# Kernel tuning notes

Hardware: AMD Instinct MI355X
Metric: run time of the kernel (lower is better)

## Reference

```python
import jax, jax.numpy as jnp
import numpy as np

B, N, DIM, H = 4, 2048, 64, 8
SCALE = DIM ** -0.5  # qk_scale defaults to head_dim**-0.5 with head_dim = dim


def setup_inputs() -> dict:
    key = jax.random.key(0)
    k1, k2, k3 = jax.random.split(key, 3)
    x = jax.random.normal(k1, (B, N, DIM), dtype=jnp.float32)
    Wqkv = jax.random.normal(k2, (DIM, 3 * H * DIM), dtype=jnp.float32) * (DIM ** -0.5)
    Wproj = jax.random.normal(k3, (H * DIM, DIM), dtype=jnp.float32) * ((H * DIM) ** -0.5)
    bproj = jnp.zeros((DIM,), dtype=jnp.float32)
    return {"x": x, "Wqkv": Wqkv, "Wproj": Wproj, "bproj": bproj}


def reference(x, Wqkv, Wproj, bproj):
    Bx, Nx, C = x.shape
    # qkv: [B,N,3*H*C] -> [B,N,3,H,C] -> (3,B,H,N,C)
    qkv = (x @ Wqkv).reshape(Bx, Nx, 3, H, C).transpose(2, 0, 3, 1, 4)
    q, k, v = qkv[0], qkv[1], qkv[2]
    # scores: [B,H,N,N]
    attn = jax.nn.softmax(jnp.einsum('bhnc,bhmc->bhnm', q, k) * SCALE, axis=-1)
    out = jnp.einsum('bhnm,bhmc->bhnc', attn, v)  # [B,H,N,C]
    out = out.transpose(0, 2, 1, 3).reshape(Bx, Nx, H * C)  # [B,N,H*C]
    return out @ Wproj + bproj  # [B,N,C]
```

## Files before the change

kernel.cpp:

```cpp
#include <hip/hip_runtime.h>

#define NB 4
#define SEQ 2048
#define CD 64
#define NHEAD 8
#define BHN (NB * NHEAD)
#define ROWS (NB * SEQ)
#define HC 512

#define QSCALE 0.18033688011112042f
#define SHIFT  23.083120654223414f

typedef float f32x4 __attribute__((ext_vector_type(4)));
typedef short s16x8 __attribute__((ext_vector_type(8)));
typedef unsigned short u16;
typedef unsigned int u32;

__device__ __forceinline__ u16 f2bf(float x) {
  union { float f; unsigned u; } v; v.f = x;
  unsigned r = v.u + 0x7FFFu + ((v.u >> 16) & 1u);
  return (u16)(r >> 16);
}

__device__ __forceinline__ float fast_exp2(float x) {
#if __has_builtin(__builtin_amdgcn_exp2f)
  return __builtin_amdgcn_exp2f(x);
#else
  return exp2f(x);
#endif
}

__device__ __forceinline__ u32 bitsf(float x) {
  union { float f; u32 u; } v; v.f = x; return v.u;
}

__device__ __forceinline__ u32 pack_trunc(float a, float b) {
#if __has_builtin(__builtin_amdgcn_perm)
  return __builtin_amdgcn_perm(bitsf(b), bitsf(a), 0x07060302u);
#else
  return (bitsf(a) >> 16) | (bitsf(b) & 0xFFFF0000u);
#endif
}

__device__ __forceinline__ f32x4 mfma_bf16(s16x8 a, s16x8 b, f32x4 c) {
  return __builtin_amdgcn_mfma_f32_16x16x32_bf16(a, b, c, 0, 0, 0);
}

typedef __attribute__((address_space(1))) const u32* gp1;
typedef __attribute__((address_space(3))) u32* lp3;
__device__ __forceinline__ void dma16(const void* g, void* l) {
  __builtin_amdgcn_global_load_lds((gp1)g, (lp3)l, 16, 0, 0);
}

__global__ void __launch_bounds__(256) prep_kernel(
    const float* __restrict__ Wqkv, const float* __restrict__ Wproj,
    u16* __restrict__ WT, u16* __restrict__ WpT) {
  const int idx = blockIdx.x * 256 + threadIdx.x;
  if (idx < 64 * 1536) {
    const int k = idx / 1536, n = idx % 1536;
    WT[n * CD + k] = f2bf(Wqkv[idx]);
  }
  if (idx < 512 * 64) {
    const int k = idx >> 6, c = idx & 63;
    WpT[c * HC + k] = f2bf(Wproj[idx]);
  }
}

__global__ void __launch_bounds__(256) qkv_kernel(
    const float* __restrict__ x, const u16* __restrict__ WT,
    u16* __restrict__ Q, u16* __restrict__ K, u16* __restrict__ Vt) {
  __shared__ __align__(16) u16 xs[64 * 72];
  __shared__ __align__(16) u16 wts[192 * 72];

  const int t = threadIdx.x;
  const int w = t >> 6, lane = t & 63, quad = lane >> 4, c16 = lane & 15;
  const int rb = blockIdx.x * 64;
  const int c0 = blockIdx.y * 192;

  {
    const int row = t >> 2, cc0 = (t & 3) * 16;
    const float* xp = x + (size_t)(rb + row) * CD + cc0;
    union { u16 u[16]; int4 v[2]; } bx;
#pragma unroll
    for (int j = 0; j < 16; j += 4) {
      float4 xv = *(const float4*)(xp + j);
      bx.u[j] = f2bf(xv.x); bx.u[j + 1] = f2bf(xv.y);
      bx.u[j + 2] = f2bf(xv.z); bx.u[j + 3] = f2bf(xv.w);
    }
    *(int4*)&xs[row * 72 + cc0] = bx.v[0];
    *(int4*)&xs[row * 72 + cc0 + 8] = bx.v[1];
  }
#pragma unroll
  for (int pass = 0; pass < 3; ++pass) {
    const int row = pass * 64 + (t >> 2), cc0 = (t & 3) * 16;
    const u16* src = WT + (size_t)(c0 + row) * CD + cc0;
    *(int4*)&wts[row * 72 + cc0] = *(const int4*)src;
    *(int4*)&wts[row * 72 + cc0 + 8] = *(const int4*)(src + 8);
  }
  __syncthreads();

  s16x8 af[2];
#pragma unroll
  for (int kc = 0; kc < 2; ++kc)
    af[kc] = *(const s16x8*)&xs[(w * 16 + c16) * 72 + kc * 32 + quad * 8];

  f32x4 acc[12];
#pragma unroll
  for (int nb = 0; nb < 12; ++nb) acc[nb] = (f32x4){0.f, 0.f, 0.f, 0.f};

#pragma unroll
  for (int nb = 0; nb < 12; ++nb) {
#pragma unroll
    for (int kc = 0; kc < 2; ++kc) {
      const s16x8 bf_ =
          *(const s16x8*)&wts[(nb * 16 + c16) * 72 + kc * 32 + quad * 8];
      acc[nb] = mfma_bf16(af[kc], bf_, acc[nb]);
    }
  }

  const int rw = rb + w * 16;
  const int b = rw >> 11;
  const int nn0 = rw & (SEQ - 1);
#pragma unroll
  for (int nb = 0; nb < 12; ++nb) {
    const int cb = c0 + nb * 16;
    const int three = cb >> 9;
    const int h = (cb >> 6) & 7;
    const int ccb = cb & 63;
    const int bhv = b * NHEAD + h;
    if (three == 2) {
      union { u16 u[4]; uint2 v; } pk;
#pragma unroll
      for (int i = 0; i < 4; ++i) pk.u[i] = f2bf(acc[nb][i]);
      const size_t off = (size_t)bhv * (SEQ * CD) + (size_t)(nn0 >> 5) * 2048 +
                         (size_t)(ccb + c16) * 32 + (rw & 31) + quad * 4;
      *(uint2*)(Vt + off) = pk.v;
    } else {
      u16* dstp = (three == 0) ? Q : K;
      const float scl = (three == 0) ? QSCALE : 1.0f;
#pragma unroll
      for (int i = 0; i < 4; ++i) {
        const int nn = nn0 + quad * 4 + i;
        dstp[((size_t)bhv * SEQ + nn) * CD + ccb + c16] = f2bf(acc[nb][i] * scl);
      }
    }
  }
}

__global__ void __launch_bounds__(128, 2) attn_kernel(
    const u16* __restrict__ Q, const u16* __restrict__ K,
    const u16* __restrict__ Vt, u16* __restrict__ O) {
  __shared__ __align__(16) u16 smem[17664];

  const int t = threadIdx.x;
  const int w = t >> 6, lane = t & 63, quad = lane >> 4, c16 = lane & 15;
  const int bh = blockIdx.y;
  const int q0 = blockIdx.x * 64;
  const int kt0 = w * (SEQ / 2);

  u16* KsW = smem + w * 8192;
  u16* VsW = smem + w * 8192 + 4096;
  u16* Pw  = smem + 16384 + w * 640;

  const u16* Qb = Q + (size_t)bh * SEQ * CD;
  const u16* Kb = K + (size_t)bh * SEQ * CD;
  const u16* Vb = Vt + (size_t)bh * SEQ * CD;

  s16x8 qfb[4][2];
#pragma unroll
  for (int qb = 0; qb < 4; ++qb)
#pragma unroll
    for (int cc = 0; cc < 2; ++cc)
      qfb[qb][cc] = *(const s16x8*)(Qb + (size_t)(q0 + qb * 16 + c16) * CD +
                                    cc * 32 + quad * 8);

  s16x8 onesf;
  {
    const short one = (c16 == 0) ? (short)0x3F80 : (short)0;
#pragma unroll
    for (int j = 0; j < 8; ++j) onesf[j] = one;
  }

  f32x4 o[4][4], osum[4];
#pragma unroll
  for (int qb = 0; qb < 4; ++qb) {
    osum[qb] = (f32x4){0.f, 0.f, 0.f, 0.f};
#pragma unroll
    for (int cb = 0; cb < 4; ++cb) o[qb][cb] = (f32x4){0.f, 0.f, 0.f, 0.f};
  }

  const int krl = lane >> 3, kcl = (lane & 7) ^ ((lane >> 3) & 7);
  const int vrl = lane >> 2, vcl = (lane & 3) ^ ((lane >> 3) & 3);

  int kOff[2][2], vOff[4];
#pragma unroll
  for (int kb = 0; kb < 2; ++kb)
#pragma unroll
    for (int cc = 0; cc < 2; ++cc)
      kOff[kb][cc] = (kb * 16 + c16) * 64 + (((cc * 4 + quad) ^ (c16 & 7)) * 8);
#pragma unroll
  for (int cb = 0; cb < 4; ++cb)
    vOff[cb] = (cb * 16 + c16) * 32 + ((quad ^ ((c16 >> 1) & 3)) * 8);

#define STAGE_TILE(buf_, kt_)                                                  \
  {                                                                            \
    const u16* ksrc = Kb + (size_t)(kt_) * CD;                                 \
    _Pragma("unroll") for (int d = 0; d < 4; ++d)                              \
        dma16(ksrc + (size_t)(d * 8 + krl) * CD + kcl * 8,                     \
              KsW + (buf_) * 2048 + d * 512);                                  \
    const u16* vsrc = Vb + (size_t)((kt_) >> 5) * 2048;                        \
    _Pragma("unroll") for (int d = 0; d < 4; ++d)                              \
        dma16(vsrc + (size_t)(d * 16 + vrl) * 32 + vcl * 8,                    \
              VsW + (buf_) * 2048 + d * 512);                                  \
  }

  STAGE_TILE(0, kt0)

  for (int it = 0; it < 32; ++it) {
    const int bs = it & 1;
    __syncthreads();

    if (it + 1 < 32) STAGE_TILE(bs ^ 1, kt0 + (it + 1) * 32)

    s16x8 kf[2][2], vf[4];
#pragma unroll
    for (int kb = 0; kb < 2; ++kb)
#pragma unroll
      for (int cc = 0; cc < 2; ++cc)
        kf[kb][cc] = *(const s16x8*)&KsW[bs * 2048 + kOff[kb][cc]];
#pragma unroll
    for (int cb = 0; cb < 4; ++cb)
      vf[cb] = *(const s16x8*)&VsW[bs * 2048 + vOff[cb]];

#pragma unroll
    for (int qb = 0; qb < 4; ++qb) {
#pragma unroll
      for (int kb = 0; kb < 2; ++kb) {
        f32x4 s = (f32x4){-SHIFT, -SHIFT, -SHIFT, -SHIFT};
        s = mfma_bf16(kf[kb][0], qfb[qb][0], s);
        s = mfma_bf16(kf[kb][1], qfb[qb][1], s);
        uint2 pk;
        pk.x = pack_trunc(fast_exp2(s[0]), fast_exp2(s[1]));
        pk.y = pack_trunc(fast_exp2(s[2]), fast_exp2(s[3]));
        *(uint2*)&Pw[c16 * 40 + kb * 16 + quad * 4] = pk;
      }
      const s16x8 pf = *(const s16x8*)&Pw[c16 * 40 + quad * 8];
#pragma unroll
      for (int cb = 0; cb < 4; ++cb)
        o[qb][cb] = mfma_bf16(pf, vf[cb], o[qb][cb]);
      osum[qb] = mfma_bf16(pf, onesf, osum[qb]);
    }
  }
#undef STAGE_TILE

  float* X  = (float*)(smem + 8192);
  float* Lx = (float*)(smem + 16384 + 640);

  if (w == 1) {
#pragma unroll
    for (int qb = 0; qb < 4; ++qb) {
#pragma unroll
      for (int cb = 0; cb < 4; ++cb)
#pragma unroll
        for (int i = 0; i < 4; ++i)
          X[(qb * 16 + quad * 4 + i) * 64 + cb * 16 + c16] = o[qb][cb][i];
      if (c16 == 0)
#pragma unroll
        for (int i = 0; i < 4; ++i)
          Lx[qb * 16 + quad * 4 + i] = osum[qb][i];
    }
  }
  __syncthreads();
  if (w == 0) {
    const int b = bh >> 3, h = bh & 7;
#pragma unroll
    for (int qb = 0; qb < 4; ++qb) {
#pragma unroll
      for (int i = 0; i < 4; ++i) {
        const float l0 = __shfl(osum[qb][i], lane & 48);
        const int qq = qb * 16 + quad * 4 + i;
        const float inv = 1.0f / (l0 + Lx[qq]);
        const int q = q0 + qq;
        u16* dst = O + ((size_t)(b * SEQ + q)) * HC + h * CD;
#pragma unroll
        for (int cb = 0; cb < 4; ++cb)
          dst[cb * 16 + c16] =
              f2bf((o[qb][cb][i] + X[qq * 64 + cb * 16 + c16]) * inv);
      }
    }
  }
}

__global__ void __launch_bounds__(256) proj_kernel(
    const u16* __restrict__ O, const u16* __restrict__ WpT,
    const float* __restrict__ bias, float* __restrict__ out) {
  __shared__ __align__(16) u16 Ls[16 * 520];
  __shared__ __align__(16) float Cred[4][64][20];
  const int t = threadIdx.x;
  const int w = t >> 6, lane = t & 63, quad = lane >> 4, c16 = lane & 15;
  const int r0 = blockIdx.x * 16;

  s16x8 wf[4][4];
#pragma unroll
  for (int kc = 0; kc < 4; ++kc)
#pragma unroll
    for (int nb = 0; nb < 4; ++nb)
      wf[kc][nb] = *(const s16x8*)(WpT + (size_t)(nb * 16 + c16) * HC +
                                   w * 128 + kc * 32 + quad * 8);

  {
    const int row = t >> 4, cg = (t & 15) * 8;
#pragma unroll
    for (int p = 0; p < 4; ++p)
      *(int4*)&Ls[row * 520 + p * 128 + cg] =
          *(const int4*)(O + (size_t)(r0 + row) * HC + p * 128 + cg);
  }
  __syncthreads();

  f32x4 acc[4];
#pragma unroll
  for (int nb = 0; nb < 4; ++nb) acc[nb] = (f32x4){0.f, 0.f, 0.f, 0.f};
#pragma unroll
  for (int kc = 0; kc < 4; ++kc) {
    const s16x8 af =
        *(const s16x8*)&Ls[c16 * 520 + w * 128 + kc * 32 + quad * 8];
#pragma unroll
    for (int nb = 0; nb < 4; ++nb)
      acc[nb] = mfma_bf16(af, wf[kc][nb], acc[nb]);
  }

#pragma unroll
  for (int nb = 0; nb < 4; ++nb)
    *(f32x4*)&Cred[w][nb * 16 + c16][quad * 4] = acc[nb];
  __syncthreads();

  const int col = t & 63, rbase = (t >> 6) * 4;
  const float bv = bias[col];
#pragma unroll
  for (int j = 0; j < 4; ++j) {
    const int r = rbase + j;
    out[(size_t)(r0 + r) * CD + col] = Cred[0][col][r] + Cred[1][col][r] +
                                       Cred[2][col][r] + Cred[3][col][r] + bv;
  }
}

extern "C" void kernel_launch(void* const* d_in, const int* in_sizes, int n_in,
                              void* d_out, int out_size, void* d_ws, size_t ws_size,
                              hipStream_t stream) {
  (void)in_sizes; (void)n_in; (void)out_size; (void)ws_size;
  const float* x     = (const float*)d_in[0];
  const float* Wqkv  = (const float*)d_in[1];
  const float* Wproj = (const float*)d_in[2];
  const float* bproj = (const float*)d_in[3];
  float* out = (float*)d_out;

  u16* WT  = (u16*)d_ws;
  u16* WpT = WT + 1536 * CD;
  u16* Qw  = WpT + CD * HC;
  u16* Kw  = Qw + (size_t)BHN * SEQ * CD;
  u16* Vtw = Kw + (size_t)BHN * SEQ * CD;
  u16* Ow  = Vtw + (size_t)BHN * SEQ * CD;

  prep_kernel<<<384, 256, 0, stream>>>(Wqkv, Wproj, WT, WpT);
  qkv_kernel<<<dim3(128, 8), 256, 0, stream>>>(x, WT, Qw, Kw, Vtw);
  attn_kernel<<<dim3(32, 32), 128, 0, stream>>>(Qw, Kw, Vtw, Ow);
  proj_kernel<<<512, 256, 0, stream>>>(Ow, WpT, bproj, out);
}
```

Before: 126.1 us.

## Fold weight prep into QKV kernel, single-buffer attention tiles, vectorize QKV stores

Removes the separate prep kernel: the QKV kernel converts and transposes the fp32 Wqkv tile into shared memory itself, and an extra block column pre-swizzles Wproj into an MFMA-fragment layout so the projection kernel can load it with contiguous lane loads. Q/K outputs are produced transposed via swapped MFMA operands so each lane writes packed 8-byte stores instead of scalar 2-byte ones. The attention kernel drops K/V double buffering and the per-iteration barrier, using explicit waitcnts to load fragments and then issue the next DMA into the same buffer, and gives each query block its own P staging area. This saves a launch and barriers but exposes load latency per tile and relies on hand-written waitcnt encodings being correct.

```diff
diff --git a/kernel.cpp b/kernel.cpp
--- a/kernel.cpp
+++ b/kernel.cpp
@@ -42,6 +42,10 @@
 #endif
 }
 
+__device__ __forceinline__ u32 pack_rne(float a, float b) {
+  return (u32)f2bf(a) | ((u32)f2bf(b) << 16);
+}
+
 __device__ __forceinline__ f32x4 mfma_bf16(s16x8 a, s16x8 b, f32x4 c) {
   return __builtin_amdgcn_mfma_f32_16x16x32_bf16(a, b, c, 0, 0, 0);
 }
@@ -52,27 +56,25 @@
   __builtin_amdgcn_global_load_lds((gp1)g, (lp3)l, 16, 0, 0);
 }
 
-__global__ void __launch_bounds__(256) prep_kernel(
-    const float* __restrict__ Wqkv, const float* __restrict__ Wproj,
-    u16* __restrict__ WT, u16* __restrict__ WpT) {
-  const int idx = blockIdx.x * 256 + threadIdx.x;
-  if (idx < 64 * 1536) {
-    const int k = idx / 1536, n = idx % 1536;
-    WT[n * CD + k] = f2bf(Wqkv[idx]);
-  }
-  if (idx < 512 * 64) {
-    const int k = idx >> 6, c = idx & 63;
-    WpT[c * HC + k] = f2bf(Wproj[idx]);
-  }
-}
-
 __global__ void __launch_bounds__(256) qkv_kernel(
-    const float* __restrict__ x, const u16* __restrict__ WT,
-    u16* __restrict__ Q, u16* __restrict__ K, u16* __restrict__ Vt) {
+    const float* __restrict__ x, const float* __restrict__ Wqkv,
+    const float* __restrict__ Wproj, u16* __restrict__ Q, u16* __restrict__ K,
+    u16* __restrict__ Vt, u16* __restrict__ WpF) {
+  const int t = threadIdx.x;
+
+  if (blockIdx.x == 128) {
+    for (int i = blockIdx.y * 256 + t; i < 64 * 512; i += 2048) {
+      const int f = i >> 9, ln = (i >> 3) & 63, j = i & 7;
+      const int col = (f & 3) * 16 + (ln & 15);
+      const int k = (f >> 2) * 32 + (ln >> 4) * 8 + j;
+      WpF[i] = f2bf(Wproj[k * 64 + col]);
+    }
+    return;
+  }
+
   __shared__ __align__(16) u16 xs[64 * 72];
   __shared__ __align__(16) u16 wts[192 * 72];
 
-  const int t = threadIdx.x;
   const int w = t >> 6, lane = t & 63, quad = lane >> 4, c16 = lane & 15;
   const int rb = blockIdx.x * 64;
   const int c0 = blockIdx.y * 192;
@@ -91,11 +93,15 @@
     *(int4*)&xs[row * 72 + cc0 + 8] = bx.v[1];
   }
 #pragma unroll
-  for (int pass = 0; pass < 3; ++pass) {
-    const int row = pass * 64 + (t >> 2), cc0 = (t & 3) * 16;
-    const u16* src = WT + (size_t)(c0 + row) * CD + cc0;
-    *(int4*)&wts[row * 72 + cc0] = *(const int4*)src;
-    *(int4*)&wts[row * 72 + cc0 + 8] = *(const int4*)(src + 8);
+  for (int p = 0; p < 12; ++p) {
+    const int idx = p * 256 + t;
+    const int n = idx % 192, k4 = (idx / 192) * 4;
+    const float* wp = Wqkv + (size_t)k4 * 1536 + c0 + n;
+    const float w0 = wp[0], w1 = wp[1536], w2 = wp[3072], w3 = wp[4608];
+    uint2 pk;
+    pk.x = pack_rne(w0, w1);
+    pk.y = pack_rne(w2, w3);
+    *(uint2*)&wts[n * 72 + k4] = pk;
   }
   __syncthreads();
 
@@ -103,24 +109,11 @@
 #pragma unroll
   for (int kc = 0; kc < 2; ++kc)
     af[kc] = *(const s16x8*)&xs[(w * 16 + c16) * 72 + kc * 32 + quad * 8];
-
-  f32x4 acc[12];
-#pragma unroll
-  for (int nb = 0; nb < 12; ++nb) acc[nb] = (f32x4){0.f, 0.f, 0.f, 0.f};
-
-#pragma unroll
-  for (int nb = 0; nb < 12; ++nb) {
-#pragma unroll
-    for (int kc = 0; kc < 2; ++kc) {
-      const s16x8 bf_ =
-          *(const s16x8*)&wts[(nb * 16 + c16) * 72 + kc * 32 + quad * 8];
-      acc[nb] = mfma_bf16(af[kc], bf_, acc[nb]);
-    }
-  }
 
   const int rw = rb + w * 16;
   const int b = rw >> 11;
   const int nn0 = rw & (SEQ - 1);
+
 #pragma unroll
   for (int nb = 0; nb < 12; ++nb) {
     const int cb = c0 + nb * 16;
@@ -128,21 +121,32 @@
     const int h = (cb >> 6) & 7;
     const int ccb = cb & 63;
     const int bhv = b * NHEAD + h;
+    s16x8 bf_[2];
+#pragma unroll
+    for (int kc = 0; kc < 2; ++kc)
+      bf_[kc] = *(const s16x8*)&wts[(nb * 16 + c16) * 72 + kc * 32 + quad * 8];
+
     if (three == 2) {
-      union { u16 u[4]; uint2 v; } pk;
-#pragma unroll
-      for (int i = 0; i < 4; ++i) pk.u[i] = f2bf(acc[nb][i]);
+      f32x4 acc = (f32x4){0.f, 0.f, 0.f, 0.f};
+#pragma unroll
+      for (int kc = 0; kc < 2; ++kc) acc = mfma_bf16(af[kc], bf_[kc], acc);
+      uint2 pk;
+      pk.x = pack_rne(acc[0], acc[1]);
+      pk.y = pack_rne(acc[2], acc[3]);
       const size_t off = (size_t)bhv * (SEQ * CD) + (size_t)(nn0 >> 5) * 2048 +
                          (size_t)(ccb + c16) * 32 + (rw & 31) + quad * 4;
-      *(uint2*)(Vt + off) = pk.v;
+      *(uint2*)(Vt + off) = pk;
     } else {
+      f32x4 acc = (f32x4){0.f, 0.f, 0.f, 0.f};
+#pragma unroll
+      for (int kc = 0; kc < 2; ++kc) acc = mfma_bf16(bf_[kc], af[kc], acc);
       u16* dstp = (three == 0) ? Q : K;
       const float scl = (three == 0) ? QSCALE : 1.0f;
-#pragma unroll
-      for (int i = 0; i < 4; ++i) {
-        const int nn = nn0 + quad * 4 + i;
-        dstp[((size_t)bhv * SEQ + nn) * CD + ccb + c16] = f2bf(acc[nb][i] * scl);
-      }
+      uint2 pk;
+      pk.x = pack_rne(acc[0] * scl, acc[1] * scl);
+      pk.y = pack_rne(acc[2] * scl, acc[3] * scl);
+      *(uint2*)(dstp + ((size_t)bhv * SEQ + nn0 + c16) * CD + ccb + quad * 4) =
+          pk;
     }
   }
 }
@@ -150,7 +154,7 @@
 __global__ void __launch_bounds__(128, 2) attn_kernel(
     const u16* __restrict__ Q, const u16* __restrict__ K,
     const u16* __restrict__ Vt, u16* __restrict__ O) {
-  __shared__ __align__(16) u16 smem[17664];
+  __shared__ __align__(16) u16 smem[13312];
 
   const int t = threadIdx.x;
   const int w = t >> 6, lane = t & 63, quad = lane >> 4, c16 = lane & 15;
@@ -158,9 +162,9 @@
   const int q0 = blockIdx.x * 64;
   const int kt0 = w * (SEQ / 2);
 
-  u16* KsW = smem + w * 8192;
-  u16* VsW = smem + w * 8192 + 4096;
-  u16* Pw  = smem + 16384 + w * 640;
+  u16* KsW = smem + w * 4096;
+  u16* VsW = smem + w * 4096 + 2048;
+  u16* Pw  = smem + 8192 + w * 2560;
 
   const u16* Qb = Q + (size_t)bh * SEQ * CD;
   const u16* Kb = K + (size_t)bh * SEQ * CD;
@@ -202,38 +206,37 @@
   for (int cb = 0; cb < 4; ++cb)
     vOff[cb] = (cb * 16 + c16) * 32 + ((quad ^ ((c16 >> 1) & 3)) * 8);
 
-#define STAGE_TILE(buf_, kt_)                                                  \
+#define STAGE_TILE(kt_)                                                        \
   {                                                                            \
     const u16* ksrc = Kb + (size_t)(kt_) * CD;                                 \
     _Pragma("unroll") for (int d = 0; d < 4; ++d)                              \
-        dma16(ksrc + (size_t)(d * 8 + krl) * CD + kcl * 8,                     \
-              KsW + (buf_) * 2048 + d * 512);                                  \
+        dma16(ksrc + (size_t)(d * 8 + krl) * CD + kcl * 8, KsW + d * 512);     \
     const u16* vsrc = Vb + (size_t)((kt_) >> 5) * 2048;                        \
     _Pragma("unroll") for (int d = 0; d < 4; ++d)                              \
-        dma16(vsrc + (size_t)(d * 16 + vrl) * 32 + vcl * 8,                    \
-              VsW + (buf_) * 2048 + d * 512);                                  \
-  }
-
-  STAGE_TILE(0, kt0)
+        dma16(vsrc + (size_t)(d * 16 + vrl) * 32 + vcl * 8, VsW + d * 512);    \
+  }
+
+  STAGE_TILE(kt0)
 
   for (int it = 0; it < 32; ++it) {
-    const int bs = it & 1;
-    __syncthreads();
-
-    if (it + 1 < 32) STAGE_TILE(bs ^ 1, kt0 + (it + 1) * 32)
+    __builtin_amdgcn_s_waitcnt(0x0F70);
 
     s16x8 kf[2][2], vf[4];
 #pragma unroll
     for (int kb = 0; kb < 2; ++kb)
 #pragma unroll
       for (int cc = 0; cc < 2; ++cc)
-        kf[kb][cc] = *(const s16x8*)&KsW[bs * 2048 + kOff[kb][cc]];
+        kf[kb][cc] = *(const s16x8*)&KsW[kOff[kb][cc]];
 #pragma unroll
     for (int cb = 0; cb < 4; ++cb)
-      vf[cb] = *(const s16x8*)&VsW[bs * 2048 + vOff[cb]];
+      vf[cb] = *(const s16x8*)&VsW[vOff[cb]];
+
+    __builtin_amdgcn_s_waitcnt(0xC07F);
+    if (it + 1 < 32) STAGE_TILE(kt0 + (it + 1) * 32)
 
 #pragma unroll
     for (int qb = 0; qb < 4; ++qb) {
+      u16* Pq = Pw + qb * 640;
 #pragma unroll
       for (int kb = 0; kb < 2; ++kb) {
         f32x4 s = (f32x4){-SHIFT, -SHIFT, -SHIFT, -SHIFT};
@@ -242,9 +245,9 @@
         uint2 pk;
         pk.x = pack_trunc(fast_exp2(s[0]), fast_exp2(s[1]));
         pk.y = pack_trunc(fast_exp2(s[2]), fast_exp2(s[3]));
-        *(uint2*)&Pw[c16 * 40 + kb * 16 + quad * 4] = pk;
+        *(uint2*)&Pq[c16 * 40 + kb * 16 + quad * 4] = pk;
       }
-      const s16x8 pf = *(const s16x8*)&Pw[c16 * 40 + quad * 8];
+      const s16x8 pf = *(const s16x8*)&Pq[c16 * 40 + quad * 8];
 #pragma unroll
       for (int cb = 0; cb < 4; ++cb)
         o[qb][cb] = mfma_bf16(pf, vf[cb], o[qb][cb]);
@@ -253,9 +256,10 @@
   }
 #undef STAGE_TILE
 
-  float* X  = (float*)(smem + 8192);
-  float* Lx = (float*)(smem + 16384 + 640);
-
+  float* X  = (float*)smem;
+  float* Lx = (float*)(smem + 8192);
+
+  __syncthreads();
   if (w == 1) {
 #pragma unroll
     for (int qb = 0; qb < 4; ++qb) {
@@ -292,7 +296,7 @@
 }
 
 __global__ void __launch_bounds__(256) proj_kernel(
-    const u16* __restrict__ O, const u16* __restrict__ WpT,
+    const u16* __restrict__ O, const u16* __restrict__ WpF,
     const float* __restrict__ bias, float* __restrict__ out) {
   __shared__ __align__(16) u16 Ls[16 * 520];
   __shared__ __align__(16) float Cred[4][64][20];
@@ -305,8 +309,8 @@
   for (int kc = 0; kc < 4; ++kc)
 #pragma unroll
     for (int nb = 0; nb < 4; ++nb)
-      wf[kc][nb] = *(const s16x8*)(WpT + (size_t)(nb * 16 + c16) * HC +
-                                   w * 128 + kc * 32 + quad * 8);
+      wf[kc][nb] = *(const s16x8*)(WpF + ((((w * 4 + kc) * 4 + nb) << 9) +
+                                          lane * 8));
 
   {
     const int row = t >> 4, cg = (t & 15) * 8;
@@ -354,15 +358,14 @@
   const float* bproj = (const float*)d_in[3];
   float* out = (float*)d_out;
 
-  u16* WT  = (u16*)d_ws;
-  u16* WpT = WT + 1536 * CD;
-  u16* Qw  = WpT + CD * HC;
+  u16* WpF = (u16*)d_ws;
+  u16* Qw  = WpF + CD * HC;
   u16* Kw  = Qw + (size_t)BHN * SEQ * CD;
   u16* Vtw = Kw + (size_t)BHN * SEQ * CD;
   u16* Ow  = Vtw + (size_t)BHN * SEQ * CD;
 
-  prep_kernel<<<384, 256, 0, stream>>>(Wqkv, Wproj, WT, WpT);
-  qkv_kernel<<<dim3(128, 8), 256, 0, stream>>>(x, WT, Qw, Kw, Vtw);
+  qkv_kernel<<<dim3(129, 8), 256, 0, stream>>>(x, Wqkv, Wproj, Qw, Kw, Vtw,
+                                               WpF);
   attn_kernel<<<dim3(32, 32), 128, 0, stream>>>(Qw, Kw, Vtw, Ow);
-  proj_kernel<<<512, 256, 0, stream>>>(Ow, WpT, bproj, out);
-}
+  proj_kernel<<<512, 256, 0, stream>>>(Ow, WpF, bproj, out);
+}
```

Result: faster. 123.5 us (-2.1%).
